# Performance work log

Measured on AMD Instinct MI355X. Metric: run time of the kernel, lower is better.

## Reference

```python
import jax, jax.numpy as jnp
import numpy as np

LOCAL_HEADS = 8
GLOBAL_HEADS = 4
HEAD_DIM = 16  # dim // local_heads


def setup_inputs() -> dict:
    key = jax.random.key(0)
    ks = jax.random.split(key, 6)
    B, N, C = 8, 1024, 128
    gdim = HEAD_DIM * GLOBAL_HEADS  # 64
    return {
        "x": jax.random.normal(ks[0], (B, N, C), dtype=jnp.float32),
        "masks": jax.random.uniform(ks[1], (N, N, 3), dtype=jnp.float32),
        "Wq": jax.random.normal(ks[2], (gdim, C), dtype=jnp.float32) * 0.05,
        "Wk": jax.random.normal(ks[3], (gdim, C), dtype=jnp.float32) * 0.05,
        "Wv": jax.random.normal(ks[4], (C, C), dtype=jnp.float32) * 0.05,
        "mask_proj": jax.random.normal(ks[5], (3, GLOBAL_HEADS * LOCAL_HEADS), dtype=jnp.float32),
    }


def reference(x, masks, Wq, Wk, Wv, mask_proj):
    B, N, C = x.shape
    # projections (torch Linear: y = x @ W.T)
    q = (x @ Wq.T).reshape(B, N, GLOBAL_HEADS, HEAD_DIM)   # [B,N,G,hd]
    k = (x @ Wk.T).reshape(B, N, GLOBAL_HEADS, HEAD_DIM)
    v = (x @ Wv.T).reshape(B, N, LOCAL_HEADS, HEAD_DIM)    # [B,N,L,hd]
    # raw global-head scores: [B,G,N,N]  (no 1/sqrt(d) scaling in original)
    attn = jnp.einsum('bigd,bjgd->bgij', q, k)
    # learned mask mixing: masks [N,N,3] @ mask_proj [3, G*L] -> [N,N,G,L]
    mw = (masks @ mask_proj).reshape(N, N, GLOBAL_HEADS, LOCAL_HEADS)
    # mix global heads into local heads: [B,L,N,N]
    scores = jnp.einsum('bgij,ijgl->blij', attn, mw)
    probs = jax.nn.softmax(scores, axis=-1)               # over keys j
    out = jnp.einsum('blij,bjld->bild', probs, v)         # [B,N,L,hd]
    return out.reshape(B, N, C)
```

## Files before the change

### kernel.cpp

```cpp
#include <hip/hip_runtime.h>

#define BB 8
#define NN 1024
#define CC 128
#define GG 4
#define LL 8
#define GD 64

typedef __attribute__((ext_vector_type(8))) short short8;
typedef __attribute__((ext_vector_type(4))) short short4v;
typedef __attribute__((ext_vector_type(4))) float floatx4;

__device__ __forceinline__ short f2b(float f) {
  union { float f; unsigned u; } c; c.f = f;
  unsigned u = c.u;
  return (short)((u + 0x7FFFu + ((u >> 16) & 1u)) >> 16);
}
__device__ __forceinline__ float b2f(short s) {
  union { unsigned u; float f; } c; c.u = ((unsigned)(unsigned short)s) << 16;
  return c.f;
}
__device__ __forceinline__ void split2(float v, short& hi, short& lo) {
  short h = f2b(v);
  hi = h;
  lo = f2b(v - b2f(h));
}

__global__ __launch_bounds__(256) void proj_kernel(
    const float* __restrict__ x, const float* __restrict__ Wq,
    const float* __restrict__ Wk, const float* __restrict__ Wv,
    short* __restrict__ qb, short* __restrict__ kb, short* __restrict__ vtb)
{
  const int t = threadIdx.x;
  const int nt = blockIdx.x & 3;
  const int mt = blockIdx.x >> 2;
  const int w = t >> 6;
  const int lane = t & 63;
  const int ln = lane & 15;
  const int hq = lane >> 4;
  const int arow = mt * 64 + w * 16 + ln;

  const float* wbase = (nt == 0) ? Wq : (nt == 1) ? Wk : (Wv + (nt - 2) * 64 * 128);
  const floatx4 zf = {0.f, 0.f, 0.f, 0.f};
  floatx4 acc[4] = {zf, zf, zf, zf};

  #pragma unroll
  for (int kc = 0; kc < 4; ++kc) {
    const float* xp = x + (long)arow * 128 + kc * 32 + hq * 8;
    float4 a0 = *(const float4*)xp;
    float4 a1 = *(const float4*)(xp + 4);
    union { short s[8]; short8 v; } Ah, Al;
    float av[8] = {a0.x,a0.y,a0.z,a0.w,a1.x,a1.y,a1.z,a1.w};
    #pragma unroll
    for (int z = 0; z < 8; ++z) split2(av[z], Ah.s[z], Al.s[z]);
    #pragma unroll
    for (int ns = 0; ns < 4; ++ns) {
      const float* wp = wbase + (long)(ns * 16 + ln) * 128 + kc * 32 + hq * 8;
      float4 b0 = *(const float4*)wp;
      float4 b1 = *(const float4*)(wp + 4);
      union { short s[8]; short8 v; } Bh, Bl;
      float bv[8] = {b0.x,b0.y,b0.z,b0.w,b1.x,b1.y,b1.z,b1.w};
      #pragma unroll
      for (int z = 0; z < 8; ++z) split2(bv[z], Bh.s[z], Bl.s[z]);
      acc[ns] = __builtin_amdgcn_mfma_f32_16x16x32_bf16(Ah.v, Bh.v, acc[ns], 0,0,0);
      acc[ns] = __builtin_amdgcn_mfma_f32_16x16x32_bf16(Al.v, Bh.v, acc[ns], 0,0,0);
      acc[ns] = __builtin_amdgcn_mfma_f32_16x16x32_bf16(Ah.v, Bl.v, acc[ns], 0,0,0);
    }
  }

  if (nt < 2) {
    short* dst = (nt == 0) ? qb : kb;
    #pragma unroll
    for (int ns = 0; ns < 4; ++ns) {
      int col = ns * 16 + ln;
      #pragma unroll
      for (int reg = 0; reg < 4; ++reg) {
        int row = mt * 64 + w * 16 + hq * 4 + reg;
        dst[(long)row * 64 + col] = f2b(acc[ns][reg]);
      }
    }
  } else {
    int b = mt >> 4;
    int tok = (mt * 64 + w * 16 + hq * 4) & 1023;
    #pragma unroll
    for (int ns = 0; ns < 4; ++ns) {
      int cv = (nt - 2) * 64 + ns * 16 + ln;
      union { short s[4]; short4v v; } o;
      #pragma unroll
      for (int reg = 0; reg < 4; ++reg) o.s[reg] = f2b(acc[ns][reg]);
      *(short4v*)(vtb + ((long)b * CC + cv) * NN + tok) = o.v;
    }
  }
}

#define IT 16
#define JT 64
#define SPLIT 4
#define JSPAN 256
#define NTL 4
#define ARP 260
#define MRP 196

__global__ __launch_bounds__(256, 3) void attn_kernel(
    const short* __restrict__ qb, const short* __restrict__ kb,
    const short* __restrict__ vtb, const float* __restrict__ masks,
    const float* __restrict__ mask_proj,
    float* __restrict__ pnum, float* __restrict__ pden3)
{
  __shared__ float arec[IT * ARP];
  __shared__ float mrec[2][IT * MRP];

  const int t = threadIdx.x;
  const int sp = blockIdx.x & 3;
  const int itile = (blockIdx.x >> 2) & 63;
  const int b = blockIdx.x >> 8;
  const int i0 = itile * IT;

  const int w = t >> 6;
  const int lane = t & 63;
  const int ln = lane & 15;
  const int hq = lane >> 4;
  const int l0 = 2 * w, l1 = 2 * w + 1;

  short8 qf;
  {
    union { short s[8]; short8 v; } qq;
    #pragma unroll
    for (int z = 0; z < 8; ++z) qq.s[z] = 0;
    if (hq < 2)
      qq.v = *(const short8*)(qb + ((long)(b * NN + i0 + ln)) * GD + w * 16 + hq * 8);
    qf = qq.v;
  }
  float ycA[3][4], ycB[3][4];
  #pragma unroll
  for (int m = 0; m < 3; ++m)
    #pragma unroll
    for (int g = 0; g < 4; ++g) {
      ycA[m][g] = mask_proj[m * 32 + g * 8 + l0];
      ycB[m][g] = mask_proj[m * 32 + g * 8 + l1];
    }

  const floatx4 zf = {0.f, 0.f, 0.f, 0.f};
  floatx4 pv0 = zf, pv1 = zf;
  float den0 = 0.f, den1 = 0.f;

  const short* kbase = kb + (long)b * NN * GD;
  const short* v0base = vtb + ((long)b * CC + l0 * 16 + ln) * NN;
  const short* v1base = vtb + ((long)b * CC + l1 * 16 + ln) * NN;

  for (int jt = 0; jt < NTL; ++jt) {
    const int j0 = sp * JSPAN + jt * JT;
    float* mrp = mrec[jt & 1];

    #pragma unroll
    for (int it2 = 0; it2 < 3; ++it2) {
      int f = t + it2 * 256;
      int ii = f / 48;
      int rem = f - ii * 48;
      *(float4*)(mrp + ii * MRP + rem * 4) =
        *(const float4*)(masks + (long)(i0 + ii) * (NN * 3) + (long)j0 * 3 + rem * 4);
    }
    __syncthreads();

    #pragma unroll
    for (int jsub = 0; jsub < 4; ++jsub) {
      union { short s[8]; short8 v; } kk;
      #pragma unroll
      for (int z = 0; z < 8; ++z) kk.s[z] = 0;
      if (hq < 2)
        kk.v = *(const short8*)(kbase + (long)(j0 + jsub * 16 + ln) * GD + w * 16 + hq * 8);
      floatx4 at = __builtin_amdgcn_mfma_f32_16x16x32_bf16(qf, kk.v, zf, 0, 0, 0);
      float* ab = arec + (jsub * 16 + ln) * 4 + w;
      #pragma unroll
      for (int reg = 0; reg < 4; ++reg)
        ab[(hq * 4 + reg) * ARP] = at[reg];
    }
    __syncthreads();

    #pragma unroll
    for (int mf = 0; mf < 2; ++mf) {
      float mku[24];
      {
        const float* mb = mrp + ln * MRP + mf * 96 + hq * 24;
        #pragma unroll
        for (int q4 = 0; q4 < 6; ++q4)
          *(float4*)(mku + q4 * 4) = *(const float4*)(mb + q4 * 4);
      }
      short8 vf0 = *(const short8*)(v0base + j0 + mf * 32 + hq * 8);
      short8 vf1 = *(const short8*)(v1base + j0 + mf * 32 + hq * 8);
      union { short s[8]; short8 v; } pA, pB;
      #pragma unroll
      for (int z = 0; z < 8; ++z) {
        floatx4 a4 = *(const floatx4*)(arec + ln * ARP + (mf * 32 + hq * 8 + z) * 4);
        float m0 = mku[z * 3], m1 = mku[z * 3 + 1], m2 = mku[z * 3 + 2];
        float wA0 = m0*ycA[0][0] + m1*ycA[1][0] + m2*ycA[2][0];
        float wA1 = m0*ycA[0][1] + m1*ycA[1][1] + m2*ycA[2][1];
        float wA2 = m0*ycA[0][2] + m1*ycA[1][2] + m2*ycA[2][2];
        float wA3 = m0*ycA[0][3] + m1*ycA[1][3] + m2*ycA[2][3];
        float wB0 = m0*ycB[0][0] + m1*ycB[1][0] + m2*ycB[2][0];
        float wB1 = m0*ycB[0][1] + m1*ycB[1][1] + m2*ycB[2][1];
        float wB2 = m0*ycB[0][2] + m1*ycB[1][2] + m2*ycB[2][2];
        float wB3 = m0*ycB[0][3] + m1*ycB[1][3] + m2*ycB[2][3];
        float scA = a4[0]*wA0 + a4[1]*wA1 + a4[2]*wA2 + a4[3]*wA3;
        float scB = a4[0]*wB0 + a4[1]*wB1 + a4[2]*wB2 + a4[3]*wB3;
        short ea = f2b(__expf(scA));
        short eb = f2b(__expf(scB));
        den0 += b2f(ea);
        den1 += b2f(eb);
        pA.s[z] = ea;
        pB.s[z] = eb;
      }
      pv0 = __builtin_amdgcn_mfma_f32_16x16x32_bf16(pA.v, vf0, pv0, 0, 0, 0);
      pv1 = __builtin_amdgcn_mfma_f32_16x16x32_bf16(pB.v, vf1, pv1, 0, 0, 0);
    }
  }

  #pragma unroll
  for (int reg = 0; reg < 4; ++reg) {
    long row = ((long)(sp * BB + b)) * NN + i0 + hq * 4 + reg;
    pnum[row * CC + l0 * 16 + ln] = pv0[reg];
    pnum[row * CC + l1 * 16 + ln] = pv1[reg];
  }
  long drow = ((long)(sp * BB + b)) * NN + i0 + ln;
  pden3[drow * 32 + l0 * 4 + hq] = den0;
  pden3[drow * 32 + l1 * 4 + hq] = den1;
}

__global__ __launch_bounds__(256) void reduce_kernel(
    const float* __restrict__ pnum, const float* __restrict__ pden3,
    float* __restrict__ out)
{
  int e4 = blockIdx.x * 256 + threadIdx.x;
  int bi = e4 >> 5;
  int l = (e4 & 31) >> 2;
  const float4* p4 = (const float4*)pnum;
  float4 n = {0.f, 0.f, 0.f, 0.f};
  float den = 0.f;
  #pragma unroll
  for (int s = 0; s < SPLIT; ++s) {
    float4 ns = p4[e4 + (long)s * (BB * NN * CC / 4)];
    n.x += ns.x; n.y += ns.y; n.z += ns.z; n.w += ns.w;
    float4 d4 = *(const float4*)(pden3 + ((long)s * BB * NN + bi) * 32 + l * 4);
    den += d4.x + d4.y + d4.z + d4.w;
  }
  float inv = 1.0f / den;
  float4 o;
  o.x = n.x * inv; o.y = n.y * inv; o.z = n.z * inv; o.w = n.w * inv;
  ((float4*)out)[e4] = o;
}

extern "C" void kernel_launch(void* const* d_in, const int* in_sizes, int n_in,
                              void* d_out, int out_size, void* d_ws, size_t ws_size,
                              hipStream_t stream) {
  const float* x         = (const float*)d_in[0];
  const float* masks     = (const float*)d_in[1];
  const float* Wq        = (const float*)d_in[2];
  const float* Wk        = (const float*)d_in[3];
  const float* Wv        = (const float*)d_in[4];
  const float* mask_proj = (const float*)d_in[5];
  float* out = (float*)d_out;

  char* wsB = (char*)d_ws;
  short* qb    = (short*)(wsB);
  short* kb    = (short*)(wsB + (1l << 20));
  short* vtb   = (short*)(wsB + (2l << 20));
  float* pnum  = (float*)(wsB + (4l << 20));
  float* pden3 = (float*)(wsB + (20l << 20));

  proj_kernel<<<512, 256, 0, stream>>>(x, Wq, Wk, Wv, qb, kb, vtb);
  attn_kernel<<<BB * (NN / IT) * SPLIT, 256, 0, stream>>>(qb, kb, vtb, masks,
                                                          mask_proj, pnum, pden3);
  reduce_kernel<<<(BB * NN * CC / 4) / 256, 256, 0, stream>>>(pnum, pden3, out);
}
```

Baseline: 138.4 us.

## Process two batches per attention block to reuse mask mixing weights

Each attention block now handles two batch elements, so the mask-derived mixing weights (masks @ mask_proj) are loaded and computed once and applied to both batches' scores. This halves the mask loads and the weight FMAs per batch. The j tile shrinks to 32 with twice as many iterations to keep shared memory small enough for an occupancy hint of 4. Exponentials switch to exp2 with log2e folded into mask_proj, and bf16 packing uses a hardware pack builtin. In exchange the grid is half as large, there are more barriers per block, and register pressure from four accumulators rises.

After: 162.3 us. 17.3% more time.

```diff
diff --git a/kernel.cpp b/kernel.cpp
--- a/kernel.cpp
+++ b/kernel.cpp
@@ -25,6 +25,23 @@
   hi = h;
   lo = f2b(v - b2f(h));
 }
+
+#if __has_builtin(__builtin_amdgcn_cvt_pk_bf16_f32)
+__device__ __forceinline__ unsigned pk2(float a, float b) {
+  auto r = __builtin_amdgcn_cvt_pk_bf16_f32(a, b);
+  unsigned u; __builtin_memcpy(&u, &r, 4); return u;
+}
+#else
+__device__ __forceinline__ unsigned pk2(float a, float b) {
+  return (unsigned)(unsigned short)f2b(a) | ((unsigned)(unsigned short)f2b(b) << 16);
+}
+#endif
+
+#if __has_builtin(__builtin_amdgcn_exp2f)
+#define EXP2(x) __builtin_amdgcn_exp2f(x)
+#else
+#define EXP2(x) exp2f(x)
+#endif
 
 __global__ __launch_bounds__(256) void proj_kernel(
     const float* __restrict__ x, const float* __restrict__ Wq,
@@ -94,26 +111,28 @@
 }
 
 #define IT 16
-#define JT 64
+#define JT 32
 #define SPLIT 4
 #define JSPAN 256
-#define NTL 4
-#define ARP 260
-#define MRP 196
-
-__global__ __launch_bounds__(256, 3) void attn_kernel(
+#define NTL 8
+#define ARP 132
+#define AR1 (IT * ARP)
+#define MRP 100
+
+__global__ __launch_bounds__(256, 4) void attn_kernel(
     const short* __restrict__ qb, const short* __restrict__ kb,
     const short* __restrict__ vtb, const float* __restrict__ masks,
     const float* __restrict__ mask_proj,
     float* __restrict__ pnum, float* __restrict__ pden3)
 {
-  __shared__ float arec[IT * ARP];
+  __shared__ float arec[2 * IT * ARP];
   __shared__ float mrec[2][IT * MRP];
 
   const int t = threadIdx.x;
   const int sp = blockIdx.x & 3;
   const int itile = (blockIdx.x >> 2) & 63;
-  const int b = blockIdx.x >> 8;
+  const int bg = blockIdx.x >> 8;
+  const int b0 = bg * 2;
   const int i0 = itile * IT;
 
   const int w = t >> 6;
@@ -122,108 +141,148 @@
   const int hq = lane >> 4;
   const int l0 = 2 * w, l1 = 2 * w + 1;
 
-  short8 qf;
-  {
+  short8 qf[2];
+  #pragma unroll
+  for (int b2 = 0; b2 < 2; ++b2) {
     union { short s[8]; short8 v; } qq;
     #pragma unroll
     for (int z = 0; z < 8; ++z) qq.s[z] = 0;
     if (hq < 2)
-      qq.v = *(const short8*)(qb + ((long)(b * NN + i0 + ln)) * GD + w * 16 + hq * 8);
-    qf = qq.v;
-  }
+      qq.v = *(const short8*)(qb + ((long)((b0 + b2) * NN + i0 + ln)) * GD + w * 16 + hq * 8);
+    qf[b2] = qq.v;
+  }
+  const float LOG2E = 1.44269504088896340736f;
   float ycA[3][4], ycB[3][4];
   #pragma unroll
   for (int m = 0; m < 3; ++m)
     #pragma unroll
     for (int g = 0; g < 4; ++g) {
-      ycA[m][g] = mask_proj[m * 32 + g * 8 + l0];
-      ycB[m][g] = mask_proj[m * 32 + g * 8 + l1];
+      ycA[m][g] = mask_proj[m * 32 + g * 8 + l0] * LOG2E;
+      ycB[m][g] = mask_proj[m * 32 + g * 8 + l1] * LOG2E;
     }
 
   const floatx4 zf = {0.f, 0.f, 0.f, 0.f};
-  floatx4 pv0 = zf, pv1 = zf;
-  float den0 = 0.f, den1 = 0.f;
-
-  const short* kbase = kb + (long)b * NN * GD;
-  const short* v0base = vtb + ((long)b * CC + l0 * 16 + ln) * NN;
-  const short* v1base = vtb + ((long)b * CC + l1 * 16 + ln) * NN;
+  floatx4 pv00 = zf, pv01 = zf, pv10 = zf, pv11 = zf;
+  float d00 = 0.f, d01 = 0.f, d10 = 0.f, d11 = 0.f;
+
+  const short* kbase0 = kb + (long)b0 * NN * GD;
+  const short* kbase1 = kb + (long)(b0 + 1) * NN * GD;
+  const short* vb00 = vtb + ((long)b0 * CC + l0 * 16 + ln) * NN;
+  const short* vb01 = vtb + ((long)b0 * CC + l1 * 16 + ln) * NN;
+  const short* vb10 = vb00 + (long)CC * NN;
+  const short* vb11 = vb01 + (long)CC * NN;
 
   for (int jt = 0; jt < NTL; ++jt) {
     const int j0 = sp * JSPAN + jt * JT;
     float* mrp = mrec[jt & 1];
 
     #pragma unroll
-    for (int it2 = 0; it2 < 3; ++it2) {
+    for (int it2 = 0; it2 < 2; ++it2) {
       int f = t + it2 * 256;
-      int ii = f / 48;
-      int rem = f - ii * 48;
-      *(float4*)(mrp + ii * MRP + rem * 4) =
-        *(const float4*)(masks + (long)(i0 + ii) * (NN * 3) + (long)j0 * 3 + rem * 4);
+      if (f < 384) {
+        int ii = f / 24;
+        int rem = f - ii * 24;
+        *(float4*)(mrp + ii * MRP + rem * 4) =
+          *(const float4*)(masks + (long)(i0 + ii) * (NN * 3) + (long)j0 * 3 + rem * 4);
+      }
     }
     __syncthreads();
 
     #pragma unroll
-    for (int jsub = 0; jsub < 4; ++jsub) {
-      union { short s[8]; short8 v; } kk;
-      #pragma unroll
-      for (int z = 0; z < 8; ++z) kk.s[z] = 0;
-      if (hq < 2)
-        kk.v = *(const short8*)(kbase + (long)(j0 + jsub * 16 + ln) * GD + w * 16 + hq * 8);
-      floatx4 at = __builtin_amdgcn_mfma_f32_16x16x32_bf16(qf, kk.v, zf, 0, 0, 0);
-      float* ab = arec + (jsub * 16 + ln) * 4 + w;
-      #pragma unroll
-      for (int reg = 0; reg < 4; ++reg)
-        ab[(hq * 4 + reg) * ARP] = at[reg];
+    for (int b2 = 0; b2 < 2; ++b2) {
+      const short* kbase = b2 ? kbase1 : kbase0;
+      #pragma unroll
+      for (int jsub = 0; jsub < 2; ++jsub) {
+        union { short s[8]; short8 v; } kk;
+        #pragma unroll
+        for (int z = 0; z < 8; ++z) kk.s[z] = 0;
+        if (hq < 2)
+          kk.v = *(const short8*)(kbase + (long)(j0 + jsub * 16 + ln) * GD + w * 16 + hq * 8);
+        floatx4 at = __builtin_amdgcn_mfma_f32_16x16x32_bf16(qf[b2], kk.v, zf, 0, 0, 0);
+        float* ab = arec + b2 * AR1 + (jsub * 16 + ln) * 4 + w;
+        #pragma unroll
+        for (int reg = 0; reg < 4; ++reg)
+          ab[(hq * 4 + reg) * ARP] = at[reg];
+      }
     }
     __syncthreads();
 
-    #pragma unroll
-    for (int mf = 0; mf < 2; ++mf) {
+    {
       float mku[24];
       {
-        const float* mb = mrp + ln * MRP + mf * 96 + hq * 24;
+        const float* mb = mrp + ln * MRP + hq * 24;
         #pragma unroll
         for (int q4 = 0; q4 < 6; ++q4)
           *(float4*)(mku + q4 * 4) = *(const float4*)(mb + q4 * 4);
       }
-      short8 vf0 = *(const short8*)(v0base + j0 + mf * 32 + hq * 8);
-      short8 vf1 = *(const short8*)(v1base + j0 + mf * 32 + hq * 8);
-      union { short s[8]; short8 v; } pA, pB;
-      #pragma unroll
-      for (int z = 0; z < 8; ++z) {
-        floatx4 a4 = *(const floatx4*)(arec + ln * ARP + (mf * 32 + hq * 8 + z) * 4);
-        float m0 = mku[z * 3], m1 = mku[z * 3 + 1], m2 = mku[z * 3 + 2];
-        float wA0 = m0*ycA[0][0] + m1*ycA[1][0] + m2*ycA[2][0];
-        float wA1 = m0*ycA[0][1] + m1*ycA[1][1] + m2*ycA[2][1];
-        float wA2 = m0*ycA[0][2] + m1*ycA[1][2] + m2*ycA[2][2];
-        float wA3 = m0*ycA[0][3] + m1*ycA[1][3] + m2*ycA[2][3];
-        float wB0 = m0*ycB[0][0] + m1*ycB[1][0] + m2*ycB[2][0];
-        float wB1 = m0*ycB[0][1] + m1*ycB[1][1] + m2*ycB[2][1];
-        float wB2 = m0*ycB[0][2] + m1*ycB[1][2] + m2*ycB[2][2];
-        float wB3 = m0*ycB[0][3] + m1*ycB[1][3] + m2*ycB[2][3];
-        float scA = a4[0]*wA0 + a4[1]*wA1 + a4[2]*wA2 + a4[3]*wA3;
-        float scB = a4[0]*wB0 + a4[1]*wB1 + a4[2]*wB2 + a4[3]*wB3;
-        short ea = f2b(__expf(scA));
-        short eb = f2b(__expf(scB));
-        den0 += b2f(ea);
-        den1 += b2f(eb);
-        pA.s[z] = ea;
-        pB.s[z] = eb;
-      }
-      pv0 = __builtin_amdgcn_mfma_f32_16x16x32_bf16(pA.v, vf0, pv0, 0, 0, 0);
-      pv1 = __builtin_amdgcn_mfma_f32_16x16x32_bf16(pB.v, vf1, pv1, 0, 0, 0);
+      short8 vf00 = *(const short8*)(vb00 + j0 + hq * 8);
+      short8 vf01 = *(const short8*)(vb01 + j0 + hq * 8);
+      short8 vf10 = *(const short8*)(vb10 + j0 + hq * 8);
+      short8 vf11 = *(const short8*)(vb11 + j0 + hq * 8);
+      const float* arA = arec + ln * ARP + hq * 32;
+      const float* arB = arec + AR1 + ln * ARP + hq * 32;
+      union PS { unsigned u[4]; short8 v; } p00, p01, p10, p11;
+      #pragma unroll
+      for (int zp = 0; zp < 4; ++zp) {
+        float e[8];
+        #pragma unroll
+        for (int zz = 0; zz < 2; ++zz) {
+          int z = zp * 2 + zz;
+          floatx4 a0 = *(const floatx4*)(arA + z * 4);
+          floatx4 a1 = *(const floatx4*)(arB + z * 4);
+          float m0 = mku[z * 3], m1 = mku[z * 3 + 1], m2 = mku[z * 3 + 2];
+          float wA0 = m0*ycA[0][0] + m1*ycA[1][0] + m2*ycA[2][0];
+          float wA1 = m0*ycA[0][1] + m1*ycA[1][1] + m2*ycA[2][1];
+          float wA2 = m0*ycA[0][2] + m1*ycA[1][2] + m2*ycA[2][2];
+          float wA3 = m0*ycA[0][3] + m1*ycA[1][3] + m2*ycA[2][3];
+          float wB0 = m0*ycB[0][0] + m1*ycB[1][0] + m2*ycB[2][0];
+          float wB1 = m0*ycB[0][1] + m1*ycB[1][1] + m2*ycB[2][1];
+          float wB2 = m0*ycB[0][2] + m1*ycB[1][2] + m2*ycB[2][2];
+          float wB3 = m0*ycB[0][3] + m1*ycB[1][3] + m2*ycB[2][3];
+          float s00 = a0[0]*wA0 + a0[1]*wA1 + a0[2]*wA2 + a0[3]*wA3;
+          float s01 = a0[0]*wB0 + a0[1]*wB1 + a0[2]*wB2 + a0[3]*wB3;
+          float s10 = a1[0]*wA0 + a1[1]*wA1 + a1[2]*wA2 + a1[3]*wA3;
+          float s11 = a1[0]*wB0 + a1[1]*wB1 + a1[2]*wB2 + a1[3]*wB3;
+          e[zz*4+0] = EXP2(s00); e[zz*4+1] = EXP2(s01);
+          e[zz*4+2] = EXP2(s10); e[zz*4+3] = EXP2(s11);
+        }
+        unsigned u00 = pk2(e[0], e[4]);
+        unsigned u01 = pk2(e[1], e[5]);
+        unsigned u10 = pk2(e[2], e[6]);
+        unsigned u11 = pk2(e[3], e[7]);
+        p00.u[zp] = u00; p01.u[zp] = u01; p10.u[zp] = u10; p11.u[zp] = u11;
+        union { unsigned u; float f; } cA, cB;
+        cA.u = u00 << 16;          d00 += cA.f;
+        cB.u = u00 & 0xffff0000u;  d00 += cB.f;
+        cA.u = u01 << 16;          d01 += cA.f;
+        cB.u = u01 & 0xffff0000u;  d01 += cB.f;
+        cA.u = u10 << 16;          d10 += cA.f;
+        cB.u = u10 & 0xffff0000u;  d10 += cB.f;
+        cA.u = u11 << 16;          d11 += cA.f;
+        cB.u = u11 & 0xffff0000u;  d11 += cB.f;
+      }
+      pv00 = __builtin_amdgcn_mfma_f32_16x16x32_bf16(p00.v, vf00, pv00, 0, 0, 0);
+      pv01 = __builtin_amdgcn_mfma_f32_16x16x32_bf16(p01.v, vf01, pv01, 0, 0, 0);
+      pv10 = __builtin_amdgcn_mfma_f32_16x16x32_bf16(p10.v, vf10, pv10, 0, 0, 0);
+      pv11 = __builtin_amdgcn_mfma_f32_16x16x32_bf16(p11.v, vf11, pv11, 0, 0, 0);
     }
   }
 
   #pragma unroll
   for (int reg = 0; reg < 4; ++reg) {
-    long row = ((long)(sp * BB + b)) * NN + i0 + hq * 4 + reg;
-    pnum[row * CC + l0 * 16 + ln] = pv0[reg];
-    pnum[row * CC + l1 * 16 + ln] = pv1[reg];
-  }
-  long drow = ((long)(sp * BB + b)) * NN + i0 + ln;
-  pden3[drow * 32 + l0 * 4 + hq] = den0;
-  pden3[drow * 32 + l1 * 4 + hq] = den1;
+    long row0 = ((long)(sp * BB + b0)) * NN + i0 + hq * 4 + reg;
+    long row1 = row0 + NN;
+    pnum[row0 * CC + l0 * 16 + ln] = pv00[reg];
+    pnum[row0 * CC + l1 * 16 + ln] = pv01[reg];
+    pnum[row1 * CC + l0 * 16 + ln] = pv10[reg];
+    pnum[row1 * CC + l1 * 16 + ln] = pv11[reg];
+  }
+  long drow0 = ((long)(sp * BB + b0)) * NN + i0 + ln;
+  long drow1 = drow0 + NN;
+  pden3[drow0 * 32 + l0 * 4 + hq] = d00;
+  pden3[drow0 * 32 + l1 * 4 + hq] = d01;
+  pden3[drow1 * 32 + l0 * 4 + hq] = d10;
+  pden3[drow1 * 32 + l1 * 4 + hq] = d11;
 }
 
 __global__ __launch_bounds__(256) void reduce_kernel(
@@ -268,7 +327,7 @@
   float* pden3 = (float*)(wsB + (20l << 20));
 
   proj_kernel<<<512, 256, 0, stream>>>(x, Wq, Wk, Wv, qb, kb, vtb);
-  attn_kernel<<<BB * (NN / IT) * SPLIT, 256, 0, stream>>>(qb, kb, vtb, masks,
-                                                          mask_proj, pnum, pden3);
+  attn_kernel<<<(SPLIT * 64) * (BB / 2), 256, 0, stream>>>(qb, kb, vtb, masks,
+                                                           mask_proj, pnum, pden3);
   reduce_kernel<<<(BB * NN * CC / 4) / 256, 256, 0, stream>>>(pnum, pden3, out);
 }
```

## Prefetch mask tiles into registers, use exp2 and packed bf16 conversion

Applied to the files above, without the earlier changes.

Replaces the double-buffered shared mask tile with a single buffer plus a register prefetch of the next tile. The next tile's global load is issued before the score computation and written to shared memory after a trailing barrier. This cuts LDS use so the launch bound can rise from 3 to 5 blocks per SM, and hides global load latency. It also folds log2(e) into the mask projection so the exponent can use a native exp2, and packs two floats into bf16 with a hardware convert instruction. The denominator now sums unrounded exponentials rather than the bf16-rounded values fed to the MFMA, which slightly changes numerics.

New measurement: 238.4 us. 1.72x slower.

```diff
diff --git a/kernel.cpp b/kernel.cpp
--- a/kernel.cpp
+++ b/kernel.cpp
@@ -25,6 +25,23 @@
   hi = h;
   lo = f2b(v - b2f(h));
 }
+
+#if __has_builtin(__builtin_amdgcn_cvt_pk_bf16_f32)
+__device__ __forceinline__ unsigned pk2(float a, float b) {
+  auto r = __builtin_amdgcn_cvt_pk_bf16_f32(a, b);
+  unsigned u; __builtin_memcpy(&u, &r, 4); return u;
+}
+#else
+__device__ __forceinline__ unsigned pk2(float a, float b) {
+  return (unsigned)(unsigned short)f2b(a) | ((unsigned)(unsigned short)f2b(b) << 16);
+}
+#endif
+
+#if __has_builtin(__builtin_amdgcn_exp2f)
+#define EXP2(x) __builtin_amdgcn_exp2f(x)
+#else
+#define EXP2(x) exp2f(x)
+#endif
 
 __global__ __launch_bounds__(256) void proj_kernel(
     const float* __restrict__ x, const float* __restrict__ Wq,
@@ -101,14 +118,14 @@
 #define ARP 260
 #define MRP 196
 
-__global__ __launch_bounds__(256, 3) void attn_kernel(
+__global__ __launch_bounds__(256, 5) void attn_kernel(
     const short* __restrict__ qb, const short* __restrict__ kb,
     const short* __restrict__ vtb, const float* __restrict__ masks,
     const float* __restrict__ mask_proj,
     float* __restrict__ pnum, float* __restrict__ pden3)
 {
   __shared__ float arec[IT * ARP];
-  __shared__ float mrec[2][IT * MRP];
+  __shared__ float mrec[IT * MRP];
 
   const int t = threadIdx.x;
   const int sp = blockIdx.x & 3;
@@ -122,6 +139,17 @@
   const int hq = lane >> 4;
   const int l0 = 2 * w, l1 = 2 * w + 1;
 
+  const float* mgp[3];
+  float* mlp[3];
+  #pragma unroll
+  for (int it2 = 0; it2 < 3; ++it2) {
+    int f = t + it2 * 256;
+    int ii = f / 48;
+    int rem = f - ii * 48;
+    mgp[it2] = masks + (long)(i0 + ii) * (NN * 3) + rem * 4;
+    mlp[it2] = mrec + ii * MRP + rem * 4;
+  }
+
   short8 qf;
   {
     union { short s[8]; short8 v; } qq;
@@ -131,13 +159,14 @@
       qq.v = *(const short8*)(qb + ((long)(b * NN + i0 + ln)) * GD + w * 16 + hq * 8);
     qf = qq.v;
   }
+  const float LOG2E = 1.44269504088896340736f;
   float ycA[3][4], ycB[3][4];
   #pragma unroll
   for (int m = 0; m < 3; ++m)
     #pragma unroll
     for (int g = 0; g < 4; ++g) {
-      ycA[m][g] = mask_proj[m * 32 + g * 8 + l0];
-      ycB[m][g] = mask_proj[m * 32 + g * 8 + l1];
+      ycA[m][g] = mask_proj[m * 32 + g * 8 + l0] * LOG2E;
+      ycB[m][g] = mask_proj[m * 32 + g * 8 + l1] * LOG2E;
     }
 
   const floatx4 zf = {0.f, 0.f, 0.f, 0.f};
@@ -148,19 +177,18 @@
   const short* v0base = vtb + ((long)b * CC + l0 * 16 + ln) * NN;
   const short* v1base = vtb + ((long)b * CC + l1 * 16 + ln) * NN;
 
+  const int jb0 = sp * JSPAN;
+  float4 mpre[3];
+
+  #pragma unroll
+  for (int it2 = 0; it2 < 3; ++it2)
+    mpre[it2] = *(const float4*)(mgp[it2] + (long)jb0 * 3);
+  #pragma unroll
+  for (int it2 = 0; it2 < 3; ++it2)
+    *(float4*)(mlp[it2]) = mpre[it2];
+
   for (int jt = 0; jt < NTL; ++jt) {
-    const int j0 = sp * JSPAN + jt * JT;
-    float* mrp = mrec[jt & 1];
-
-    #pragma unroll
-    for (int it2 = 0; it2 < 3; ++it2) {
-      int f = t + it2 * 256;
-      int ii = f / 48;
-      int rem = f - ii * 48;
-      *(float4*)(mrp + ii * MRP + rem * 4) =
-        *(const float4*)(masks + (long)(i0 + ii) * (NN * 3) + (long)j0 * 3 + rem * 4);
-    }
-    __syncthreads();
+    const int j0 = jb0 + jt * JT;
 
     #pragma unroll
     for (int jsub = 0; jsub < 4; ++jsub) {
@@ -175,44 +203,62 @@
       for (int reg = 0; reg < 4; ++reg)
         ab[(hq * 4 + reg) * ARP] = at[reg];
     }
+
+    {
+      const long jn3 = (long)(jt + 1 < NTL ? j0 + JT : j0) * 3;
+      #pragma unroll
+      for (int it2 = 0; it2 < 3; ++it2)
+        mpre[it2] = *(const float4*)(mgp[it2] + jn3);
+    }
     __syncthreads();
 
     #pragma unroll
     for (int mf = 0; mf < 2; ++mf) {
       float mku[24];
       {
-        const float* mb = mrp + ln * MRP + mf * 96 + hq * 24;
+        const float* mb = mrec + ln * MRP + mf * 96 + hq * 24;
         #pragma unroll
         for (int q4 = 0; q4 < 6; ++q4)
           *(float4*)(mku + q4 * 4) = *(const float4*)(mb + q4 * 4);
       }
       short8 vf0 = *(const short8*)(v0base + j0 + mf * 32 + hq * 8);
       short8 vf1 = *(const short8*)(v1base + j0 + mf * 32 + hq * 8);
-      union { short s[8]; short8 v; } pA, pB;
-      #pragma unroll
-      for (int z = 0; z < 8; ++z) {
-        floatx4 a4 = *(const floatx4*)(arec + ln * ARP + (mf * 32 + hq * 8 + z) * 4);
-        float m0 = mku[z * 3], m1 = mku[z * 3 + 1], m2 = mku[z * 3 + 2];
-        float wA0 = m0*ycA[0][0] + m1*ycA[1][0] + m2*ycA[2][0];
-        float wA1 = m0*ycA[0][1] + m1*ycA[1][1] + m2*ycA[2][1];
-        float wA2 = m0*ycA[0][2] + m1*ycA[1][2] + m2*ycA[2][2];
-        float wA3 = m0*ycA[0][3] + m1*ycA[1][3] + m2*ycA[2][3];
-        float wB0 = m0*ycB[0][0] + m1*ycB[1][0] + m2*ycB[2][0];
-        float wB1 = m0*ycB[0][1] + m1*ycB[1][1] + m2*ycB[2][1];
-        float wB2 = m0*ycB[0][2] + m1*ycB[1][2] + m2*ycB[2][2];
-        float wB3 = m0*ycB[0][3] + m1*ycB[1][3] + m2*ycB[2][3];
-        float scA = a4[0]*wA0 + a4[1]*wA1 + a4[2]*wA2 + a4[3]*wA3;
-        float scB = a4[0]*wB0 + a4[1]*wB1 + a4[2]*wB2 + a4[3]*wB3;
-        short ea = f2b(__expf(scA));
-        short eb = f2b(__expf(scB));
-        den0 += b2f(ea);
-        den1 += b2f(eb);
-        pA.s[z] = ea;
-        pB.s[z] = eb;
+      const float* arA = arec + ln * ARP + (mf * 32 + hq * 8) * 4;
+      union { unsigned u[4]; short8 v; } p0, p1;
+      #pragma unroll
+      for (int zp = 0; zp < 4; ++zp) {
+        float eA[2], eB[2];
+        #pragma unroll
+        for (int zz = 0; zz < 2; ++zz) {
+          int z = zp * 2 + zz;
+          floatx4 a4 = *(const floatx4*)(arA + z * 4);
+          float m0 = mku[z * 3], m1 = mku[z * 3 + 1], m2 = mku[z * 3 + 2];
+          float wA0 = m0*ycA[0][0] + m1*ycA[1][0] + m2*ycA[2][0];
+          float wA1 = m0*ycA[0][1] + m1*ycA[1][1] + m2*ycA[2][1];
+          float wA2 = m0*ycA[0][2] + m1*ycA[1][2] + m2*ycA[2][2];
+          float wA3 = m0*ycA[0][3] + m1*ycA[1][3] + m2*ycA[2][3];
+          float wB0 = m0*ycB[0][0] + m1*ycB[1][0] + m2*ycB[2][0];
+          float wB1 = m0*ycB[0][1] + m1*ycB[1][1] + m2*ycB[2][1];
+          float wB2 = m0*ycB[0][2] + m1*ycB[1][2] + m2*ycB[2][2];
+          float wB3 = m0*ycB[0][3] + m1*ycB[1][3] + m2*ycB[2][3];
+          float sA = a4[0]*wA0 + a4[1]*wA1 + a4[2]*wA2 + a4[3]*wA3;
+          float sB = a4[0]*wB0 + a4[1]*wB1 + a4[2]*wB2 + a4[3]*wB3;
+          eA[zz] = EXP2(sA);
+          eB[zz] = EXP2(sB);
+        }
+        den0 += eA[0] + eA[1];
+        den1 += eB[0] + eB[1];
+        p0.u[zp] = pk2(eA[0], eA[1]);
+        p1.u[zp] = pk2(eB[0], eB[1]);
       }
-      pv0 = __builtin_amdgcn_mfma_f32_16x16x32_bf16(pA.v, vf0, pv0, 0, 0, 0);
-      pv1 = __builtin_amdgcn_mfma_f32_16x16x32_bf16(pB.v, vf1, pv1, 0, 0, 0);
-    }
+      pv0 = __builtin_amdgcn_mfma_f32_16x16x32_bf16(p0.v, vf0, pv0, 0, 0, 0);
+      pv1 = __builtin_amdgcn_mfma_f32_16x16x32_bf16(p1.v, vf1, pv1, 0, 0, 0);
+    }
+    __syncthreads();
+
+    #pragma unroll
+    for (int it2 = 0; it2 < 3; ++it2)
+      *(float4*)(mlp[it2]) = mpre[it2];
   }
 
   #pragma unroll
```
